# Kernel optimization log

Measured on AMD Instinct MI355X. Metric: run time of the kernel, lower is better.

Reference implementation:

```python
import jax, jax.numpy as jnp
import numpy as np

# WikiText-103 adaptive softmax config
CUTOFFS = (0, 20000, 40000, 200000, 267735)  # cluster boundaries


def setup_inputs() -> dict:
    key = jax.random.key(0)
    ks = jax.random.split(key, 12)
    N, D = 1024, 1024
    rn = lambda k, shape, std: jax.random.normal(k, shape, jnp.float32) * std
    return {
        "hidden": jax.random.normal(ks[0], (N, D), jnp.float32),
        "target": jax.random.randint(ks[1], (N,), 0, CUTOFFS[-1], jnp.int32),
        "head_w": rn(ks[2], (20000, 1024), 0.02),
        "head_b": jnp.zeros((20000,), jnp.float32),
        "cluster_w": rn(ks[3], (3, 1024), 0.02),
        "cluster_b": jnp.zeros((3,), jnp.float32),
        "proj0": rn(ks[4], (1024, 1024), 0.01),
        "proj1": rn(ks[5], (1024, 256), 0.01),
        "proj2": rn(ks[6], (1024, 64), 0.01),
        "proj3": rn(ks[7], (1024, 16), 0.01),
        "w1": rn(ks[8], (20000, 256), 0.02),
        "b1": jnp.zeros((20000,), jnp.float32),
        "w2": rn(ks[9], (160000, 64), 0.02),
        "b2": jnp.zeros((160000,), jnp.float32),
        "w3": rn(ks[10], (67735, 16), 0.02),
        "b3": jnp.zeros((67735,), jnp.float32),
    }


def _logit(h, w, b, proj):
    # F.linear(F.linear(h, proj.t()), w, b) == (h @ proj) @ w.T + b
    return (h @ proj) @ w.T + b


def reference(hidden, target, head_w, head_b, cluster_w, cluster_b,
              proj0, proj1, proj2, proj3, w1, b1, w2, b2, w3, b3):
    # head: shortlist vocab (20000) + 3 cluster logits -> [N, 20003]
    hw = jnp.concatenate([head_w, cluster_w], axis=0)
    hb = jnp.concatenate([head_b, cluster_b], axis=0)
    head_lp = jax.nn.log_softmax(_logit(hidden, hw, hb, proj0), axis=-1)

    # cluster 0 (shortlist): logprob directly from head
    t0 = jnp.clip(target, 0, CUTOFFS[1] - 1)
    lp = jnp.take_along_axis(head_lp, t0[:, None].astype(jnp.int32), axis=1)[:, 0]

    tails = [(w1, b1, proj1), (w2, b2, proj2), (w3, b3, proj3)]
    for i, (w, b, p) in enumerate(tails, start=1):
        l, r = CUTOFFS[i], CUTOFFS[i + 1]
        mask = (target >= l) & (target < r)
        ti = jnp.clip(target - l, 0, r - l - 1)
        tail_lp = jax.nn.log_softmax(_logit(hidden, w, b, p), axis=-1)  # [N, r-l]
        # note: torch code indexes head_logprob[:, -i] (reversed cluster order quirk)
        lpi = head_lp[:, -i] + jnp.take_along_axis(tail_lp, ti[:, None], axis=1)[:, 0]
        lp = jnp.where(mask, lpi, lp)

    return -lp  # nll per token, keep_order semantics
```

## Files before the change

kernel.cpp:

```cpp
#include <hip/hip_runtime.h>
#include <math.h>

typedef __bf16 bf16;
typedef __bf16 bf16x4 __attribute__((ext_vector_type(4)));
typedef __bf16 bf16x8 __attribute__((ext_vector_type(8)));
typedef float  f32x4  __attribute__((ext_vector_type(4)));

__device__ __forceinline__ f32x4 mfma16x16x32(bf16x8 a, bf16x8 b, f32x4 c) {
  return __builtin_amdgcn_mfma_f32_16x16x32_bf16(a, b, c, 0, 0, 0);
}

__device__ __forceinline__ void async16(const bf16* gp, bf16* lp) {
  __builtin_amdgcn_global_load_lds(
      (const __attribute__((address_space(1))) void*)gp,
      (__attribute__((address_space(3))) void*)lp, 16, 0, 0);
}

__global__ void __launch_bounds__(256) convert_bf16_kernel(const float* __restrict__ in,
                                                           bf16* __restrict__ out, int n4) {
  int i = blockIdx.x * 256 + threadIdx.x;
  if (i < n4) {
    float4 f = ((const float4*)in)[i];
    bf16x4 b = {(bf16)f.x, (bf16)f.y, (bf16)f.z, (bf16)f.w};
    ((bf16x4*)out)[i] = b;
  }
}

__global__ void __launch_bounds__(256) convert_pad_kernel(const float* __restrict__ in,
                                                          bf16* __restrict__ out,
                                                          int n4, int n4tot) {
  int i = blockIdx.x * 256 + threadIdx.x;
  if (i >= n4tot) return;
  bf16x4 b = {(bf16)0.f, (bf16)0.f, (bf16)0.f, (bf16)0.f};
  if (i < n4) {
    float4 f = ((const float4*)in)[i];
    b = (bf16x4){(bf16)f.x, (bf16)f.y, (bf16)f.z, (bf16)f.w};
  }
  ((bf16x4*)out)[i] = b;
}

__global__ void __launch_bounds__(256) convert_w3_kernel(const float* __restrict__ w3,
                                                         bf16* __restrict__ W3b,
                                                         int n4, int n4tot) {
  int i = blockIdx.x * 256 + threadIdx.x;
  if (i >= n4tot) return;
  int row = i >> 2, kq = i & 3;
  bf16x4 z = {(bf16)0.f, (bf16)0.f, (bf16)0.f, (bf16)0.f};
  bf16x4 b = z;
  if (i < n4) {
    float4 f = *(const float4*)&w3[(size_t)i * 4];
    b = (bf16x4){(bf16)f.x, (bf16)f.y, (bf16)f.z, (bf16)f.w};
  }
  *(bf16x4*)&W3b[(size_t)row * 32 + kq * 4] = b;
  *(bf16x4*)&W3b[(size_t)row * 32 + 16 + kq * 4] = z;
}

__global__ void __launch_bounds__(256) transpose_convert_kernel(const float* __restrict__ P,
                                                                bf16* __restrict__ Pt, int dX) {
  __shared__ float t[32][33];
  int tx = threadIdx.x & 31, ty = threadIdx.x >> 5;
  int k0 = blockIdx.x * 32, c0 = blockIdx.y * 32;
#pragma unroll
  for (int s = 0; s < 4; ++s) {
    int k = k0 + ty + s * 8, col = c0 + tx;
    t[ty + s * 8][tx] = (col < dX) ? P[(size_t)k * dX + col] : 0.f;
  }
  __syncthreads();
#pragma unroll
  for (int s = 0; s < 4; ++s) {
    int colo = c0 + ty + s * 8;
    Pt[(size_t)colo * 1024 + k0 + tx] = (bf16)t[tx][ty + s * 8];
  }
}

__global__ void __launch_bounds__(1024) compact_kernel(const int* __restrict__ target,
                                                       int* __restrict__ rowmap,
                                                       int* __restrict__ slotmap,
                                                       int* __restrict__ counts) {
  __shared__ int cnt[3];
  int tid = threadIdx.x;
  if (tid < 3) cnt[tid] = 0;
  for (int i = tid; i < 3 * 1152; i += 1024) rowmap[i] = 0;
  __syncthreads();
  int t = target[tid];
  int c = (t >= 200000) ? 2 : (t >= 40000) ? 1 : (t >= 20000) ? 0 : -1;
  int slot = -1;
  if (c >= 0) {
    slot = atomicAdd(&cnt[c], 1);
    rowmap[c * 1152 + slot] = tid;
  }
  slotmap[tid] = slot;
  __syncthreads();
  if (tid < 3) counts[tid] = cnt[tid];
}

template <int KDIM, bool LSE>
__global__ void __launch_bounds__(256) gemm_kernel(
    const bf16* __restrict__ A, int strideA,
    const int* __restrict__ rmap, const int* __restrict__ cntp,
    const bf16* __restrict__ B,
    const float* __restrict__ bias, const float* __restrict__ bias2,
    int splice, int V, float* __restrict__ part, int nchunk,
    bf16* __restrict__ Out, int strideOut, int dX) {
  constexpr int BK = (KDIM < 64) ? KDIM : 64;
  constexpr int KG = BK / 8;
  constexpr int NIT = KDIM / BK;
  __shared__ bf16 Alds[128 * BK];
  __shared__ bf16 Blds[128 * BK];
  __shared__ float wpart[2][128];

  const int tid = threadIdx.x;
  const int w = tid >> 6, lane = tid & 63;
  const int q = lane >> 4, c = lane & 15;
  const int wr = w >> 1, wc = w & 1;

  int f = blockIdx.x;
  int xr = f & 7, rb = (f >> 3) & 7, cq = f >> 6;
  int chunk = cq * 8 + xr;
  if (chunk >= nchunk) return;
  const int row0 = rb * 128, col0 = chunk * 128;
  if (cntp && row0 >= *cntp) return;

  int arow[KG / 2];
#pragma unroll
  for (int i = 0; i < KG / 2; ++i) {
    int g = i * 256 + tid;
    int r = row0 + g / KG;
    arow[i] = rmap ? rmap[r] : r;
  }

  f32x4 acc[4][4] = {};

  for (int kt = 0; kt < NIT; ++kt) {
    const int k0 = kt * BK;
#pragma unroll
    for (int i = 0; i < KG / 2; ++i) {
      int g = i * 256 + tid;
      int col = g / KG, j = g % KG;
      int kg = (KG == 8) ? (j ^ (col & 7)) : (j ^ ((col >> 1) & 3));
      bf16* abase = &Alds[(size_t)(g & ~63) * 8];
      bf16* bbase = &Blds[(size_t)(g & ~63) * 8];
      async16(A + (size_t)arow[i] * strideA + k0 + kg * 8, abase);
      async16(B + (size_t)(col0 + col) * KDIM + k0 + kg * 8, bbase);
    }
    __syncthreads();
#pragma unroll
    for (int ks = 0; ks < BK / 32; ++ks) {
      bf16x8 af[4], bfr[4];
#pragma unroll
      for (int rt = 0; rt < 4; ++rt) {
        int rl = wr * 64 + rt * 16 + c;
        int kq = ks * 4 + q;
        int kg = (KG == 8) ? (kq ^ (rl & 7)) : (kq ^ ((rl >> 1) & 3));
        af[rt] = *(const bf16x8*)&Alds[((size_t)rl * KG + kg) * 8];
      }
#pragma unroll
      for (int ct = 0; ct < 4; ++ct) {
        int cl = wc * 64 + ct * 16 + c;
        int kq = ks * 4 + q;
        int kg = (KG == 8) ? (kq ^ (cl & 7)) : (kq ^ ((cl >> 1) & 3));
        bfr[ct] = *(const bf16x8*)&Blds[((size_t)cl * KG + kg) * 8];
      }
#pragma unroll
      for (int rt = 0; rt < 4; ++rt)
#pragma unroll
        for (int ct = 0; ct < 4; ++ct)
          acc[rt][ct] = mfma16x16x32(af[rt], bfr[ct], acc[rt][ct]);
    }
    __syncthreads();
  }

  if (!LSE) {
#pragma unroll
    for (int rt = 0; rt < 4; ++rt)
#pragma unroll
      for (int ct = 0; ct < 4; ++ct)
#pragma unroll
        for (int r = 0; r < 4; ++r) {
          int col = col0 + wc * 64 + ct * 16 + c;
          if (col < dX) {
            int row = row0 + wr * 64 + rt * 16 + q * 4 + r;
            Out[(size_t)row * strideOut + col] = (bf16)acc[rt][ct][r];
          }
        }
    return;
  }

  float bv[4];
#pragma unroll
  for (int ct = 0; ct < 4; ++ct) {
    int colg = col0 + wc * 64 + ct * 16 + c;
    bv[ct] = (colg < V) ? ((colg < splice) ? bias[colg] : bias2[colg - splice]) : -INFINITY;
  }
#pragma unroll
  for (int rt = 0; rt < 4; ++rt) {
#pragma unroll
    for (int r = 0; r < 4; ++r) {
      float s = 0.f;
#pragma unroll
      for (int ct = 0; ct < 4; ++ct) s += __expf(acc[rt][ct][r] + bv[ct]);
#pragma unroll
      for (int off = 1; off <= 8; off <<= 1) s += __shfl_xor(s, off);
      if (c == 0) wpart[wc][wr * 64 + rt * 16 + q * 4 + r] = s;
    }
  }
  __syncthreads();
  if (tid < 128)
    part[(size_t)chunk * 1024 + row0 + tid] = __logf(wpart[0][tid] + wpart[1][tid]);
}

template <int KDIM, int G>
__global__ void __launch_bounds__(256) gemm_lse_wide_kernel(
    const bf16* __restrict__ A, int strideA,
    const int* __restrict__ rmap, const int* __restrict__ cntp,
    const bf16* __restrict__ B, const float* __restrict__ bias,
    int V, float* __restrict__ part, int nchunk) {
  constexpr int BK = KDIM;
  constexpr int KG = BK / 8;
  __shared__ bf16 Alds[128 * BK];
  __shared__ bf16 Blds[2][128 * BK];
  __shared__ float spart[2][2][128];

  const int tid = threadIdx.x;
  const int w = tid >> 6, lane = tid & 63;
  const int q = lane >> 4, c = lane & 15;
  const int wr = w >> 1, wc = w & 1;

  const int row0 = blockIdx.y * 128;
  if (row0 >= *cntp) return;
  const int chunk0 = blockIdx.x * G;
  const int nc = (nchunk - chunk0 < G) ? (nchunk - chunk0) : G;

#pragma unroll
  for (int i = 0; i < KG / 2; ++i) {
    int g = i * 256 + tid;
    int row = g / KG, j = g % KG;
    int kg = (KG == 8) ? (j ^ (row & 7)) : (j ^ ((row >> 1) & 3));
    int ar = rmap[row0 + row];
    async16(A + (size_t)ar * strideA + kg * 8, &Alds[(size_t)(g & ~63) * 8]);
  }
#pragma unroll
  for (int i = 0; i < KG / 2; ++i) {
    int g = i * 256 + tid;
    int col = g / KG, j = g % KG;
    int kg = (KG == 8) ? (j ^ (col & 7)) : (j ^ ((col >> 1) & 3));
    async16(B + (size_t)(chunk0 * 128 + col) * KDIM + kg * 8,
            &Blds[0][(size_t)(g & ~63) * 8]);
  }
  __syncthreads();

  bf16x8 af[BK / 32][4];
#pragma unroll
  for (int ks = 0; ks < BK / 32; ++ks)
#pragma unroll
    for (int rt = 0; rt < 4; ++rt) {
      int rl = wr * 64 + rt * 16 + c;
      int kq = ks * 4 + q;
      int kg = (KG == 8) ? (kq ^ (rl & 7)) : (kq ^ ((rl >> 1) & 3));
      af[ks][rt] = *(const bf16x8*)&Alds[((size_t)rl * KG + kg) * 8];
    }

  for (int ci = 0; ci < nc; ++ci) {
    if (ci + 1 < nc) {
#pragma unroll
      for (int i = 0; i < KG / 2; ++i) {
        int g = i * 256 + tid;
        int col = g / KG, j = g % KG;
        int kg = (KG == 8) ? (j ^ (col & 7)) : (j ^ ((col >> 1) & 3));
        async16(B + (size_t)((chunk0 + ci + 1) * 128 + col) * KDIM + kg * 8,
                &Blds[(ci + 1) & 1][(size_t)(g & ~63) * 8]);
      }
    }

    const bf16* Bl = &Blds[ci & 1][0];
    f32x4 acc[4][4] = {};
#pragma unroll
    for (int ks = 0; ks < BK / 32; ++ks) {
      bf16x8 bfr[4];
#pragma unroll
      for (int ct = 0; ct < 4; ++ct) {
        int cl = wc * 64 + ct * 16 + c;
        int kq = ks * 4 + q;
        int kg = (KG == 8) ? (kq ^ (cl & 7)) : (kq ^ ((cl >> 1) & 3));
        bfr[ct] = *(const bf16x8*)&Bl[((size_t)cl * KG + kg) * 8];
      }
#pragma unroll
      for (int rt = 0; rt < 4; ++rt)
#pragma unroll
        for (int ct = 0; ct < 4; ++ct)
          acc[rt][ct] = mfma16x16x32(af[ks][rt], bfr[ct], acc[rt][ct]);
    }

    const int col0 = (chunk0 + ci) * 128;
    float bv[4];
#pragma unroll
    for (int ct = 0; ct < 4; ++ct) {
      int colg = col0 + wc * 64 + ct * 16 + c;
      bv[ct] = (colg < V) ? bias[colg] : -INFINITY;
    }
#pragma unroll
    for (int rt = 0; rt < 4; ++rt) {
#pragma unroll
      for (int r = 0; r < 4; ++r) {
        float s = 0.f;
#pragma unroll
        for (int ct = 0; ct < 4; ++ct) s += __expf(acc[rt][ct][r] + bv[ct]);
#pragma unroll
        for (int off = 1; off <= 8; off <<= 1) s += __shfl_xor(s, off);
        if (c == 0) spart[ci & 1][wc][wr * 64 + rt * 16 + q * 4 + r] = s;
      }
    }
    __syncthreads();
    if (tid < 128)
      part[(size_t)(chunk0 + ci) * 1024 + row0 + tid] =
          __logf(spart[ci & 1][0][tid] + spart[ci & 1][1][tid]);
  }
}

__device__ __forceinline__ float wave_sum64(float v) {
#pragma unroll
  for (int off = 1; off < 64; off <<= 1) v += __shfl_xor(v, off);
  return v;
}
__device__ float lse_cm(const float* __restrict__ p, int n, int idx) {
  int lane = threadIdx.x & 63;
  float s = 0.f;
  for (int i = lane; i < n; i += 64) s += __expf(p[(size_t)i * 1024 + idx]);
  s = wave_sum64(s);
  return __logf(s);
}
__device__ float dot_bw(const bf16* __restrict__ h, const float* __restrict__ wv, int K) {
  int lane = threadIdx.x & 63;
  float s = 0.f;
  for (int i = lane; i < K; i += 64) s += (float)h[i] * wv[i];
  return wave_sum64(s);
}

__global__ void __launch_bounds__(256) final_kernel(
    const int* __restrict__ target, const int* __restrict__ slotmap,
    const float* __restrict__ pH, const float* __restrict__ p1,
    const float* __restrict__ p2, const float* __restrict__ p3,
    const bf16* __restrict__ Hcat,
    const float* __restrict__ head_w, const float* __restrict__ head_b,
    const float* __restrict__ cluster_w, const float* __restrict__ cluster_b,
    const float* __restrict__ w1, const float* __restrict__ b1,
    const float* __restrict__ w2, const float* __restrict__ b2,
    const float* __restrict__ w3, const float* __restrict__ b3,
    float* __restrict__ out) {
  int wv = threadIdx.x >> 6, lane = threadIdx.x & 63;
  int row = blockIdx.x * 4 + wv;
  int t = target[row];
  const bf16* h0 = Hcat + (size_t)row * 1408;

  float lseH = lse_cm(pH, 157, row);
  float lp;
  if (t < 20000) {
    float sel = dot_bw(h0, head_w + (size_t)t * 1024, 1024) + head_b[t];
    lp = sel - lseH;
  } else {
    int i, L, KW, nch, hoff;
    const float* pp; const float* W; const float* Bb;
    if (t < 40000)        { i = 1; L = 20000;  KW = 256; nch = 157;  hoff = 1024; pp = p1; W = w1; Bb = b1; }
    else if (t < 200000)  { i = 2; L = 40000;  KW = 64;  nch = 1250; hoff = 1280; pp = p2; W = w2; Bb = b2; }
    else                  { i = 3; L = 200000; KW = 16;  nch = 530;  hoff = 1344; pp = p3; W = w3; Bb = b3; }
    int slot = slotmap[row];
    float lseT = lse_cm(pp, nch, slot);
    int ti = t - L;
    float tsel = dot_bw(h0 + hoff, W + (size_t)ti * KW, KW) + Bb[ti];
    int j = 3 - i;
    float csel = dot_bw(h0, cluster_w + (size_t)j * 1024, 1024) + cluster_b[j];
    lp = (csel - lseH) + (tsel - lseT);
  }
  if (lane == 0) out[row] = -lp;
}

extern "C" void kernel_launch(void* const* d_in, const int* in_sizes, int n_in,
                              void* d_out, int out_size, void* d_ws, size_t ws_size,
                              hipStream_t stream) {
  (void)in_sizes; (void)n_in; (void)out_size; (void)ws_size;
  const float* hidden    = (const float*)d_in[0];
  const int*   target    = (const int*)d_in[1];
  const float* head_w    = (const float*)d_in[2];
  const float* head_b    = (const float*)d_in[3];
  const float* cluster_w = (const float*)d_in[4];
  const float* cluster_b = (const float*)d_in[5];
  const float* proj0     = (const float*)d_in[6];
  const float* proj1     = (const float*)d_in[7];
  const float* proj2     = (const float*)d_in[8];
  const float* proj3     = (const float*)d_in[9];
  const float* w1 = (const float*)d_in[10];
  const float* b1 = (const float*)d_in[11];
  const float* w2 = (const float*)d_in[12];
  const float* b2 = (const float*)d_in[13];
  const float* w3 = (const float*)d_in[14];
  const float* b3 = (const float*)d_in[15];
  float* out = (float*)d_out;

  char* p = (char*)d_ws;
  bf16* hid_b = (bf16*)p; p += (size_t)1024 * 1024 * 2;
  bf16* Hcat  = (bf16*)p; p += (size_t)1024 * 1408 * 2;
  bf16* Pcat  = (bf16*)p; p += (size_t)1408 * 1024 * 2;
  bf16* Wh    = (bf16*)p; p += (size_t)20096 * 1024 * 2;
  bf16* W1b   = (bf16*)p; p += (size_t)20096 * 256 * 2;
  bf16* W2b   = (bf16*)p; p += (size_t)160000 * 64 * 2;
  bf16* W3b   = (bf16*)p; p += (size_t)67840 * 32 * 2;
  float* pH   = (float*)p; p += (size_t)157 * 1024 * 4;
  float* p1   = (float*)p; p += (size_t)157 * 1024 * 4;
  float* p2   = (float*)p; p += (size_t)1250 * 1024 * 4;
  float* p3   = (float*)p; p += (size_t)530 * 1024 * 4;
  int* rowmap = (int*)p;  p += 3 * 1152 * 4;
  int* slotmap= (int*)p;  p += 1024 * 4;
  int* counts = (int*)p;  p += 3 * 4;

  compact_kernel<<<1, 1024, 0, stream>>>(target, rowmap, slotmap, counts);

  convert_bf16_kernel<<<1024, 256, 0, stream>>>(hidden, hid_b, 262144);
  convert_bf16_kernel<<<20000, 256, 0, stream>>>(head_w, Wh, 5120000);
  convert_pad_kernel<<<96, 256, 0, stream>>>(cluster_w, Wh + (size_t)20000 * 1024, 768, 24576);
  convert_pad_kernel<<<5024, 256, 0, stream>>>(w1, W1b, 1280000, 1286144);
  convert_bf16_kernel<<<10000, 256, 0, stream>>>(w2, W2b, 2560000);
  convert_w3_kernel<<<1060, 256, 0, stream>>>(w3, W3b, 270940, 271360);
  transpose_convert_kernel<<<dim3(32, 32), 256, 0, stream>>>(proj0, Pcat, 1024);
  transpose_convert_kernel<<<dim3(32, 8), 256, 0, stream>>>(proj1, Pcat + (size_t)1024 * 1024, 256);
  transpose_convert_kernel<<<dim3(32, 2), 256, 0, stream>>>(proj2, Pcat + (size_t)1280 * 1024, 64);
  transpose_convert_kernel<<<dim3(32, 1), 256, 0, stream>>>(proj3, Pcat + (size_t)1344 * 1024, 16);

  gemm_kernel<1024, false><<<128, 256, 0, stream>>>(hid_b, 1024, nullptr, nullptr, Pcat,
                                                    nullptr, nullptr, 0, 0, nullptr, 11,
                                                    Hcat, 1408, 1376);

  gemm_kernel<1024, true><<<64 * 20, 256, 0, stream>>>(Hcat, 1408, nullptr, nullptr, Wh,
                                                       head_b, cluster_b, 20000, 20003,
                                                       pH, 157, nullptr, 0, 0);
  gemm_kernel<256, true><<<64 * 20, 256, 0, stream>>>(Hcat + 1024, 1408, rowmap, counts, W1b,
                                                      b1, b1, 0x40000000, 20000,
                                                      p1, 157, nullptr, 0, 0);

  gemm_lse_wide_kernel<64, 4><<<dim3(313, 8), 256, 0, stream>>>(
      Hcat + 1280, 1408, rowmap + 1152, counts + 1, W2b, b2, 160000, p2, 1250);
  gemm_lse_wide_kernel<32, 2><<<dim3(265, 8), 256, 0, stream>>>(
      Hcat + 1344, 1408, rowmap + 2304, counts + 2, W3b, b3, 67735, p3, 530);

  final_kernel<<<256, 256, 0, stream>>>(target, slotmap, pH, p1, p2, p3, Hcat,
                                        head_w, head_b, cluster_w, cluster_b,
                                        w1, b1, w2, b2, w3, b3, out);
}
```

Measured before the change: 428.1 us.

## Triple-buffer wide LSE kernel, accumulate sums in registers, write one partial per block

The wide tail GEMM+LSE kernel moves to a three-stage B buffer with explicit vmcnt waits and a raw barrier. Bias values are preloaded into LDS, and exp-sums are kept in registers across chunks, so the cross-lane reduction and partial write happen once per block instead of once per chunk. Chunks per block grow to 8, which shrinks the grid and the number of partials that the final kernel reduces. The trade-offs are fewer blocks, and therefore less parallelism for the small tail GEMMs, plus more LDS per block. Redundant prefetches of the last chunk near the tail add a little extra traffic.

Measured after the change: 397.0 us. 1.08x faster.

```diff
diff --git a/kernel.cpp b/kernel.cpp
--- a/kernel.cpp
+++ b/kernel.cpp
@@ -217,9 +217,11 @@
     int V, float* __restrict__ part, int nchunk) {
   constexpr int BK = KDIM;
   constexpr int KG = BK / 8;
+  constexpr int NL = KG / 2;
   __shared__ bf16 Alds[128 * BK];
-  __shared__ bf16 Blds[2][128 * BK];
-  __shared__ float spart[2][2][128];
+  __shared__ bf16 Blds[3][128 * BK];
+  __shared__ float biasl[G * 128];
+  __shared__ float spart[2][128];
 
   const int tid = threadIdx.x;
   const int w = tid >> 6, lane = tid & 63;
@@ -231,8 +233,12 @@
   const int chunk0 = blockIdx.x * G;
   const int nc = (nchunk - chunk0 < G) ? (nchunk - chunk0) : G;
 
-#pragma unroll
-  for (int i = 0; i < KG / 2; ++i) {
+  for (int i = tid; i < G * 128; i += 256) {
+    int colg = chunk0 * 128 + i;
+    biasl[i] = (colg < V) ? bias[colg] : -INFINITY;
+  }
+#pragma unroll
+  for (int i = 0; i < NL; ++i) {
     int g = i * 256 + tid;
     int row = g / KG, j = g % KG;
     int kg = (KG == 8) ? (j ^ (row & 7)) : (j ^ ((row >> 1) & 3));
@@ -240,12 +246,16 @@
     async16(A + (size_t)ar * strideA + kg * 8, &Alds[(size_t)(g & ~63) * 8]);
   }
 #pragma unroll
-  for (int i = 0; i < KG / 2; ++i) {
-    int g = i * 256 + tid;
-    int col = g / KG, j = g % KG;
-    int kg = (KG == 8) ? (j ^ (col & 7)) : (j ^ ((col >> 1) & 3));
-    async16(B + (size_t)(chunk0 * 128 + col) * KDIM + kg * 8,
-            &Blds[0][(size_t)(g & ~63) * 8]);
+  for (int b = 0; b < 2; ++b) {
+    int ck = (b < nc) ? b : nc - 1;
+#pragma unroll
+    for (int i = 0; i < NL; ++i) {
+      int g = i * 256 + tid;
+      int col = g / KG, j = g % KG;
+      int kg = (KG == 8) ? (j ^ (col & 7)) : (j ^ ((col >> 1) & 3));
+      async16(B + (size_t)((chunk0 + ck) * 128 + col) * KDIM + kg * 8,
+              &Blds[b][(size_t)(g & ~63) * 8]);
+    }
   }
   __syncthreads();
 
@@ -260,19 +270,24 @@
       af[ks][rt] = *(const bf16x8*)&Alds[((size_t)rl * KG + kg) * 8];
     }
 
+  float sums[4][4] = {};
+  int ib = 0;
+
   for (int ci = 0; ci < nc; ++ci) {
-    if (ci + 1 < nc) {
-#pragma unroll
-      for (int i = 0; i < KG / 2; ++i) {
+    {
+      int pre = (ci + 2 < nc) ? ci + 2 : nc - 1;
+      bf16* bw = Blds[(ib == 0) ? 2 : ib - 1];
+#pragma unroll
+      for (int i = 0; i < NL; ++i) {
         int g = i * 256 + tid;
         int col = g / KG, j = g % KG;
         int kg = (KG == 8) ? (j ^ (col & 7)) : (j ^ ((col >> 1) & 3));
-        async16(B + (size_t)((chunk0 + ci + 1) * 128 + col) * KDIM + kg * 8,
-                &Blds[(ci + 1) & 1][(size_t)(g & ~63) * 8]);
+        async16(B + (size_t)((chunk0 + pre) * 128 + col) * KDIM + kg * 8,
+                &bw[(size_t)(g & ~63) * 8]);
       }
     }
 
-    const bf16* Bl = &Blds[ci & 1][0];
+    const bf16* Bl = Blds[ib];
     f32x4 acc[4][4] = {};
 #pragma unroll
     for (int ks = 0; ks < BK / 32; ++ks) {
@@ -291,30 +306,37 @@
           acc[rt][ct] = mfma16x16x32(af[ks][rt], bfr[ct], acc[rt][ct]);
     }
 
-    const int col0 = (chunk0 + ci) * 128;
     float bv[4];
 #pragma unroll
-    for (int ct = 0; ct < 4; ++ct) {
-      int colg = col0 + wc * 64 + ct * 16 + c;
-      bv[ct] = (colg < V) ? bias[colg] : -INFINITY;
-    }
-#pragma unroll
-    for (int rt = 0; rt < 4; ++rt) {
+    for (int ct = 0; ct < 4; ++ct) bv[ct] = biasl[ci * 128 + wc * 64 + ct * 16 + c];
+#pragma unroll
+    for (int rt = 0; rt < 4; ++rt)
 #pragma unroll
       for (int r = 0; r < 4; ++r) {
-        float s = 0.f;
-#pragma unroll
-        for (int ct = 0; ct < 4; ++ct) s += __expf(acc[rt][ct][r] + bv[ct]);
-#pragma unroll
-        for (int off = 1; off <= 8; off <<= 1) s += __shfl_xor(s, off);
-        if (c == 0) spart[ci & 1][wc][wr * 64 + rt * 16 + q * 4 + r] = s;
+#pragma unroll
+        for (int ct = 0; ct < 4; ++ct)
+          sums[rt][r] += __expf(acc[rt][ct][r] + bv[ct]);
       }
-    }
-    __syncthreads();
-    if (tid < 128)
-      part[(size_t)(chunk0 + ci) * 1024 + row0 + tid] =
-          __logf(spart[ci & 1][0][tid] + spart[ci & 1][1][tid]);
-  }
+
+    if constexpr (NL == 4) asm volatile("s_waitcnt vmcnt(4)" ::: "memory");
+    else                   asm volatile("s_waitcnt vmcnt(2)" ::: "memory");
+    __builtin_amdgcn_sched_barrier(0);
+    __builtin_amdgcn_s_barrier();
+    ib = (ib == 2) ? 0 : ib + 1;
+  }
+
+#pragma unroll
+  for (int rt = 0; rt < 4; ++rt)
+#pragma unroll
+    for (int r = 0; r < 4; ++r) {
+      float s = sums[rt][r];
+#pragma unroll
+      for (int off = 1; off <= 8; off <<= 1) s += __shfl_xor(s, off);
+      if (c == 0) spart[wc][wr * 64 + rt * 16 + q * 4 + r] = s;
+    }
+  __syncthreads();
+  if (tid < 128)
+    part[(size_t)blockIdx.x * 1024 + row0 + tid] = __logf(spart[0][tid] + spart[1][tid]);
 }
 
 __device__ __forceinline__ float wave_sum64(float v) {
@@ -360,9 +382,9 @@
   } else {
     int i, L, KW, nch, hoff;
     const float* pp; const float* W; const float* Bb;
-    if (t < 40000)        { i = 1; L = 20000;  KW = 256; nch = 157;  hoff = 1024; pp = p1; W = w1; Bb = b1; }
-    else if (t < 200000)  { i = 2; L = 40000;  KW = 64;  nch = 1250; hoff = 1280; pp = p2; W = w2; Bb = b2; }
-    else                  { i = 3; L = 200000; KW = 16;  nch = 530;  hoff = 1344; pp = p3; W = w3; Bb = b3; }
+    if (t < 40000)        { i = 1; L = 20000;  KW = 256; nch = 157; hoff = 1024; pp = p1; W = w1; Bb = b1; }
+    else if (t < 200000)  { i = 2; L = 40000;  KW = 64;  nch = 157; hoff = 1280; pp = p2; W = w2; Bb = b2; }
+    else                  { i = 3; L = 200000; KW = 16;  nch = 67;  hoff = 1344; pp = p3; W = w3; Bb = b3; }
     int slot = slotmap[row];
     float lseT = lse_cm(pp, nch, slot);
     int ti = t - L;
@@ -436,9 +458,9 @@
                                                       b1, b1, 0x40000000, 20000,
                                                       p1, 157, nullptr, 0, 0);
 
-  gemm_lse_wide_kernel<64, 4><<<dim3(313, 8), 256, 0, stream>>>(
+  gemm_lse_wide_kernel<64, 8><<<dim3(157, 8), 256, 0, stream>>>(
       Hcat + 1280, 1408, rowmap + 1152, counts + 1, W2b, b2, 160000, p2, 1250);
-  gemm_lse_wide_kernel<32, 2><<<dim3(265, 8), 256, 0, stream>>>(
+  gemm_lse_wide_kernel<32, 8><<<dim3(67, 8), 256, 0, stream>>>(
       Hcat + 1344, 1408, rowmap + 2304, counts + 2, W3b, b3, 67735, p3, 530);
 
   final_kernel<<<256, 256, 0, stream>>>(target, slotmap, pH, p1, p2, p3, Hcat,
```
